# Performance work log

Hardware: AMD Instinct MI355X
Metric: run time of the kernel (lower is better)

Reference implementation:

```python
import jax, jax.numpy as jnp
import numpy as np
from jax.ops import segment_sum

N = 100000
E = 3200000
IN_DIM = 256
OUT_DIM = 64
LN_EPS = 1e-5
NEG_SLOPE = 0.01


def setup_inputs() -> dict:
    key = jax.random.key(0)
    k1, k2, k3, k4, k5 = jax.random.split(key, 5)
    x = jax.random.normal(k1, (N, IN_DIM), dtype=jnp.float32)
    edge_index = jax.random.randint(k2, (2, E), 0, N, dtype=jnp.int32)
    edge_weight = jax.random.uniform(k3, (E,), dtype=jnp.float32)
    # GCNConv params (glorot-ish scale) + LayerNorm params
    W = jax.random.normal(k4, (IN_DIM, OUT_DIM), dtype=jnp.float32) / np.sqrt(IN_DIM)
    b = jnp.zeros((OUT_DIM,), dtype=jnp.float32)
    gamma = jnp.ones((OUT_DIM,), dtype=jnp.float32)
    beta = jnp.zeros((OUT_DIM,), dtype=jnp.float32)
    return {"x": x, "edge_index": edge_index, "edge_weight": edge_weight,
            "W": W, "b": b, "gamma": gamma, "beta": beta}


def _gcn_forward(x, edge_index, edge_weight, W, b, gamma, beta):
    n = x.shape[0]
    # add self-loops with weight 1 (PyG GCNConv default)
    loops = jnp.arange(n, dtype=edge_index.dtype)
    src = jnp.concatenate([edge_index[0], loops])   # [E+N] message sources
    dst = jnp.concatenate([edge_index[1], loops])   # [E+N] aggregation targets
    ew = jnp.concatenate([edge_weight, jnp.ones((n,), dtype=edge_weight.dtype)])
    # symmetric normalization: deg computed on dst via weighted scatter
    deg = segment_sum(ew, dst, num_segments=n)                   # [N]
    dinv = jnp.where(deg > 0, jax.lax.rsqrt(deg), 0.0)           # deg^{-1/2}
    norm = dinv[src] * ew * dinv[dst]                            # [E+N]
    h = x @ W                                                    # [N, OUT]
    agg = segment_sum(h[src] * norm[:, None], dst, num_segments=n)  # [N, OUT]
    y = agg + b
    # leaky_relu then LayerNorm over last dim
    y = jnp.where(y >= 0, y, NEG_SLOPE * y)
    mu = jnp.mean(y, axis=-1, keepdims=True)
    var = jnp.mean(jnp.square(y - mu), axis=-1, keepdims=True)
    return (y - mu) * jax.lax.rsqrt(var + LN_EPS) * gamma + beta


def reference(x, edge_index, edge_weight, W, b, gamma, beta):
    return _gcn_forward(x, edge_index, edge_weight, W, b, gamma, beta)
```

## Files before the change

kernel.cpp:

```cpp
#include <hip/hip_runtime.h>

#define NN 100000
#define NE 3200000
#define OVCAP 65536

#define BINSZ 64
#define NBIN ((NN + BINSZ - 1) / BINSZ)
#define MAXPB 4096
#define SCAT_BLOCKS 512

struct OvEnt { int dst; int src; float ew; int pad; };


__global__ void k_zero(int* __restrict__ bincnt, int* __restrict__ ovcnt, int n) {
    int i = blockIdx.x * 256 + threadIdx.x;
    if (i < n) bincnt[i] = 0;
    if (i == 0) *ovcnt = 0;
}

__global__ __launch_bounds__(256) void k_binscatter(
    const int* __restrict__ src, const int* __restrict__ dst,
    const float* __restrict__ ew, int* __restrict__ bincnt,
    uint2* __restrict__ binbuf, int cap,
    OvEnt* __restrict__ ov, int* __restrict__ ovcnt, int e) {
    __shared__ int hist[NBIN];
    int t = threadIdx.x;
    int chunk = (e + gridDim.x - 1) / gridDim.x;
    int beg = blockIdx.x * chunk;
    int end = beg + chunk; if (end > e) end = e;
    for (int j = t; j < NBIN; j += 256) hist[j] = 0;
    __syncthreads();
    for (int i = beg + t; i < end; i += 256)
        atomicAdd(&hist[dst[i] >> 6], 1);
    __syncthreads();
    for (int j = t; j < NBIN; j += 256) {
        int c = hist[j];
        hist[j] = (c > 0) ? atomicAdd(&bincnt[j], c) : 0;
    }
    __syncthreads();
    for (int i = beg + t; i < end; i += 256) {
        int s = src[i], d = dst[i];
        float w = ew[i];
        int bin = d >> 6;
        int pos = atomicAdd(&hist[bin], 1);
        if (pos < cap) {
            unsigned key = (unsigned)s | ((unsigned)(d & 63) << 17);
            binbuf[(size_t)bin * cap + pos] = make_uint2(key, __float_as_uint(w));
        } else {
            int op = atomicAdd(ovcnt, 1);
            if (op < OVCAP) { OvEnt t2; t2.dst = d; t2.src = s; t2.ew = w; t2.pad = 0; ov[op] = t2; }
        }
    }
}

__global__ __launch_bounds__(256) void k_binsort(
    const int* __restrict__ bincnt, uint2* __restrict__ binbuf, int cap,
    const OvEnt* __restrict__ ov, const int* __restrict__ ovcnt,
    float* __restrict__ dinv, int* __restrict__ off, int* __restrict__ ncnt,
    int* __restrict__ binov, int n) {
    __shared__ float sdeg[BINSZ];
    __shared__ int hcnt[BINSZ];
    __shared__ int hoff[BINSZ];
    __shared__ int sov;
    __shared__ uint2 sbuf[MAXPB];
    int bin = blockIdx.x, t = threadIdx.x;
    if (t < BINSZ) { sdeg[t] = 0.f; hcnt[t] = 0; }
    if (t == 0) {
        int c = bincnt[bin];
        sov = (c > cap);
        binov[bin] = (c > cap);
    }
    __syncthreads();
    int cnt = bincnt[bin];
    int bc = cnt < cap ? cnt : cap;
    uint2* base = binbuf + (size_t)bin * cap;
    uint2 ent[16];
    int ne = 0;
#pragma unroll
    for (int p = 0; p < 16; p++) {
        int idx = t + p * 256;
        if (idx < bc) { ent[p] = base[idx]; ne = p + 1; }
    }
#pragma unroll
    for (int p = 0; p < 16; p++) {
        if (p < ne) {
            int dl = (int)((ent[p].x >> 17) & 63u);
            atomicAdd(&hcnt[dl], 1);
            atomicAdd(&sdeg[dl], __uint_as_float(ent[p].y));
        }
    }
    if (sov) {
        int on = *ovcnt; if (on > OVCAP) on = OVCAP;
        for (int j = t; j < on; j += 256) {
            OvEnt e2 = ov[j];
            if ((e2.dst >> 6) == bin) atomicAdd(&sdeg[e2.dst & 63], e2.ew);
        }
    }
    __syncthreads();
    if (t < 64) {
        int v = hcnt[t];
        int inc = v;
#pragma unroll
        for (int o2 = 1; o2 < 64; o2 <<= 1) {
            int u = __shfl_up(inc, o2, 64);
            if (t >= o2) inc += u;
        }
        int excl = inc - v;
        hoff[t] = excl;
        int g = bin * BINSZ + t;
        if (g < n) {
            dinv[g] = rsqrtf(1.0f + sdeg[t]);
            off[g] = bin * cap + excl;
            ncnt[g] = v;
        }
    }
    __syncthreads();
#pragma unroll
    for (int p = 0; p < 16; p++) {
        if (p < ne) {
            int dl = (int)((ent[p].x >> 17) & 63u);
            int pos = atomicAdd(&hoff[dl], 1);
            sbuf[pos] = ent[p];
        }
    }
    __syncthreads();
    for (int j = t; j < bc; j += 256) base[j] = sbuf[j];
}

__global__ __launch_bounds__(256) void k_gather_s(
    const float* __restrict__ h, const float* __restrict__ dinv,
    const int* __restrict__ binov,
    const int* __restrict__ off, const int* __restrict__ ncnt,
    const uint2* __restrict__ sorted,
    const OvEnt* __restrict__ ov, const int* __restrict__ ovcnt,
    const float* __restrict__ bias, const float* __restrict__ gamma,
    const float* __restrict__ beta, float* __restrict__ out, int n) {
    int lane = threadIdx.x & 63, wid = threadIdx.x >> 6;
    int node = blockIdx.x * 4 + wid;
    if (node >= n) return;
    float di = dinv[node];
    float acc = h[(size_t)node * 64 + lane] * di * di;
    int beg = off[node], c0 = ncnt[node];
    for (int j = 0; j < c0; j += 64) {
        int c = c0 - j; if (c > 64) c = 64;
        int s = 0; float w = 0.f;
        if (lane < c) {
            uint2 v = sorted[beg + j + lane];
            s = (int)(v.x & 0x1FFFFu);
            w = __uint_as_float(v.y) * dinv[s] * di;
        }
        int i2 = 0;
        for (; i2 + 16 <= c; i2 += 16) {
            float hv[16], wv[16];
#pragma unroll
            for (int q = 0; q < 16; q++) {
                int si = __shfl(s, i2 + q, 64);
                wv[q] = __shfl(w, i2 + q, 64);
                hv[q] = h[(size_t)si * 64 + lane];
            }
#pragma unroll
            for (int q = 0; q < 16; q++) acc += hv[q] * wv[q];
        }
        if (i2 < c) {
            float hv[16], wv[16];
            int rem = c - i2;
#pragma unroll
            for (int q = 0; q < 16; q++) {
                if (q < rem) {
                    int si = __shfl(s, i2 + q, 64);
                    wv[q] = __shfl(w, i2 + q, 64);
                    hv[q] = h[(size_t)si * 64 + lane];
                } else { wv[q] = 0.f; hv[q] = 0.f; }
            }
#pragma unroll
            for (int q = 0; q < 16; q++) acc += hv[q] * wv[q];
        }
    }
    if (binov[node >> 6]) {
        int on = *ovcnt; if (on > OVCAP) on = OVCAP;
        for (int j = 0; j < on; j++) {
            OvEnt ent = ov[j];
            if (ent.dst == node)
                acc += h[(size_t)ent.src * 64 + lane] * dinv[ent.src] * ent.ew * di;
        }
    }
    float y = acc + bias[lane];
    y = (y >= 0.f) ? y : 0.01f * y;
    float sum = y;
#pragma unroll
    for (int o = 32; o > 0; o >>= 1) sum += __shfl_xor(sum, o, 64);
    float mu = sum * (1.0f / 64.0f);
    float d = y - mu;
    float v = d * d;
#pragma unroll
    for (int o = 32; o > 0; o >>= 1) v += __shfl_xor(v, o, 64);
    v *= (1.0f / 64.0f);
    out[(size_t)node * 64 + lane] = d * rsqrtf(v + 1e-5f) * gamma[lane] + beta[lane];
}

#define GR 64
#define GKC 32
#define XS_STRIDE 36
__global__ __launch_bounds__(256) void k_gemm(const float* __restrict__ x,
                                              const float* __restrict__ W,
                                              float* __restrict__ h, int n) {
    __shared__ float xs[GR][XS_STRIDE];
    __shared__ float wsh[GKC][64];
    int t = threadIdx.x;
    int tx = t & 15;
    int ty = t >> 4;
    int rbase = blockIdx.x * GR;
    float acc[4][4];
#pragma unroll
    for (int i = 0; i < 4; i++)
#pragma unroll
        for (int j = 0; j < 4; j++) acc[i][j] = 0.0f;

    for (int k0 = 0; k0 < 256; k0 += GKC) {
        const float4* wsrc = (const float4*)(W + k0 * 64);
        float4* wdst = (float4*)(&wsh[0][0]);
        wdst[t] = wsrc[t];
        wdst[t + 256] = wsrc[t + 256];
#pragma unroll
        for (int p = 0; p < 2; p++) {
            int f4 = p * 256 + t;
            int r = f4 >> 3;
            int kq = (f4 & 7) << 2;
            int row = rbase + r;
            float4 val = make_float4(0.f, 0.f, 0.f, 0.f);
            if (row < n) val = *(const float4*)(x + (size_t)row * 256 + k0 + kq);
            *(float4*)(&xs[r][kq]) = val;
        }
        __syncthreads();
        int r0 = ty * 4, c0 = tx * 4;
#pragma unroll
        for (int kk = 0; kk < GKC; kk += 4) {
            float4 wv[4];
#pragma unroll
            for (int m = 0; m < 4; m++) wv[m] = *(const float4*)(&wsh[kk + m][c0]);
#pragma unroll
            for (int i = 0; i < 4; i++) {
                float4 xv = *(const float4*)(&xs[r0 + i][kk]);
                acc[i][0] += xv.x * wv[0].x + xv.y * wv[1].x + xv.z * wv[2].x + xv.w * wv[3].x;
                acc[i][1] += xv.x * wv[0].y + xv.y * wv[1].y + xv.z * wv[2].y + xv.w * wv[3].y;
                acc[i][2] += xv.x * wv[0].z + xv.y * wv[1].z + xv.z * wv[2].z + xv.w * wv[3].z;
                acc[i][3] += xv.x * wv[0].w + xv.y * wv[1].w + xv.z * wv[2].w + xv.w * wv[3].w;
            }
        }
        __syncthreads();
    }
    int r0 = ty * 4, c0 = tx * 4;
#pragma unroll
    for (int i = 0; i < 4; i++) {
        int row = rbase + r0 + i;
        if (row < n) {
            float4 v = make_float4(acc[i][0], acc[i][1], acc[i][2], acc[i][3]);
            *(float4*)(h + (size_t)row * 64 + c0) = v;
        }
    }
}


__global__ void k_init(float* __restrict__ deg, int* __restrict__ cnt, int n) {
    int i = blockIdx.x * 256 + threadIdx.x;
    if (i < n) { deg[i] = 1.0f; cnt[i] = 0; }
}

__global__ void k_deg(const int* __restrict__ dst, const float* __restrict__ ew,
                      float* __restrict__ deg, int* __restrict__ cnt, int e) {
    int i = blockIdx.x * 256 + threadIdx.x;
    if (i < e) {
        int d = dst[i];
        atomicAdd(&deg[d], ew[i]);
        atomicAdd(&cnt[d], 1);
    }
}

#define SCAN_T 256
#define SCAN_E 8
__global__ void k_scan_blocks(const int* __restrict__ cnt, int* __restrict__ off,
                              int* __restrict__ bsum, int n) {
    __shared__ int sdata[SCAN_T];
    int base = blockIdx.x * (SCAN_T * SCAN_E);
    int t = threadIdx.x;
    int v[SCAN_E];
    int local = 0;
    int idx0 = base + t * SCAN_E;
#pragma unroll
    for (int i = 0; i < SCAN_E; i++) {
        int idx = idx0 + i;
        int c = (idx < n) ? cnt[idx] : 0;
        v[i] = local;
        local += c;
    }
    sdata[t] = local;
    __syncthreads();
    for (int o = 1; o < SCAN_T; o <<= 1) {
        int x = 0;
        if (t >= o) x = sdata[t - o];
        __syncthreads();
        sdata[t] += x;
        __syncthreads();
    }
    int excl = sdata[t] - local;
#pragma unroll
    for (int i = 0; i < SCAN_E; i++) {
        int idx = idx0 + i;
        if (idx < n) off[idx] = excl + v[i];
    }
    if (t == SCAN_T - 1) bsum[blockIdx.x] = sdata[t];
}

__global__ void k_scan_bsums(int* __restrict__ bsum, int nb) {
    int t = threadIdx.x;
    int v = (t < nb) ? bsum[t] : 0;
    int orig = v;
#pragma unroll
    for (int o = 1; o < 64; o <<= 1) {
        int u = __shfl_up(v, o, 64);
        if (t >= o) v += u;
    }
    if (t < nb) bsum[t] = v - orig;
}

__global__ void k_finalize(int* __restrict__ off, const int* __restrict__ bsum,
                           int* __restrict__ cursor, float* __restrict__ deg,
                           int n, int total) {
    int i = blockIdx.x * 256 + threadIdx.x;
    if (i < n) {
        int o = off[i] + bsum[i >> 11];
        off[i] = o;
        cursor[i] = o;
        deg[i] = rsqrtf(deg[i]);
    }
    if (i == 0) off[n] = total;
}

__global__ void k_scatter(const int* __restrict__ src, const int* __restrict__ dst,
                          const float* __restrict__ ew, const float* __restrict__ dinv,
                          int* __restrict__ cursor, int* __restrict__ ssrc,
                          float* __restrict__ snorm, int e) {
    int i = blockIdx.x * 256 + threadIdx.x;
    if (i < e) {
        int s = src[i], d = dst[i];
        float nm = dinv[s] * ew[i] * dinv[d];
        int pos = atomicAdd(&cursor[d], 1);
        ssrc[pos] = s;
        snorm[pos] = nm;
    }
}

__global__ __launch_bounds__(256) void k_gather(
    const float* __restrict__ h, const float* __restrict__ dinv,
    const int* __restrict__ off, const int* __restrict__ ssrc,
    const float* __restrict__ snorm, const float* __restrict__ bias,
    const float* __restrict__ gamma, const float* __restrict__ beta,
    float* __restrict__ out, int n) {
    int lane = threadIdx.x & 63;
    int wid = threadIdx.x >> 6;
    int node = blockIdx.x * 4 + wid;
    if (node >= n) return;
    float di = dinv[node];
    float acc = h[(size_t)node * 64 + lane] * di * di;
    int beg = off[node], end = off[node + 1];
    for (int j = beg; j < end; j += 64) {
        int cnt = end - j;
        if (cnt > 64) cnt = 64;
        int s = 0;
        float w = 0.f;
        if (lane < cnt) { s = ssrc[j + lane]; w = snorm[j + lane]; }
        for (int i2 = 0; i2 < cnt; i2++) {
            int si = __shfl(s, i2, 64);
            float wi = __shfl(w, i2, 64);
            acc += h[(size_t)si * 64 + lane] * wi;
        }
    }
    float y = acc + bias[lane];
    y = (y >= 0.f) ? y : 0.01f * y;
    float sum = y;
#pragma unroll
    for (int o = 32; o > 0; o >>= 1) sum += __shfl_xor(sum, o, 64);
    float mu = sum * (1.0f / 64.0f);
    float d = y - mu;
    float v = d * d;
#pragma unroll
    for (int o = 32; o > 0; o >>= 1) v += __shfl_xor(v, o, 64);
    v *= (1.0f / 64.0f);
    out[(size_t)node * 64 + lane] = d * rsqrtf(v + 1e-5f) * gamma[lane] + beta[lane];
}


extern "C" void kernel_launch(void* const* d_in, const int* in_sizes, int n_in,
                              void* d_out, int out_size, void* d_ws, size_t ws_size,
                              hipStream_t stream) {
    const float* x = (const float*)d_in[0];
    const int* ei = (const int*)d_in[1];
    const float* ew = (const float*)d_in[2];
    const float* W = (const float*)d_in[3];
    const float* b = (const float*)d_in[4];
    const float* gamma = (const float*)d_in[5];
    const float* beta = (const float*)d_in[6];
    float* out = (float*)d_out;

    const int n = NN, e = NE;
    const int* src = ei;
    const int* dst = ei + e;

    char* ws = (char*)d_ws;
    size_t o = 0;
    auto alloc = [&](size_t bytes) -> char* {
        char* r = ws + o;
        o = (o + bytes + 255) & ~(size_t)255;
        return r;
    };
    auto pad = [](size_t bytes) -> size_t { return (bytes + 255) & ~(size_t)255; };

    int nb_n = (n + 255) / 256;
    int nb_e = (e + 255) / 256;
    int nb_gemm = (n + GR - 1) / GR;
    int nb_w = (n + 3) / 4;

    size_t fixed = 0;
    fixed += pad((size_t)NBIN * 4);
    fixed += 256;
    fixed += pad((size_t)OVCAP * 16);
    fixed += pad((size_t)n * 4);
    fixed += pad((size_t)n * 4);
    fixed += pad((size_t)n * 4);
    fixed += pad((size_t)NBIN * 4);
    fixed += pad((size_t)n * 64 * 4);

    int cap = 0;
    if (ws_size >= fixed + pad((size_t)NBIN * 4096 * 8) + 1024) cap = 4096;
    else if (ws_size >= fixed + pad((size_t)NBIN * 3072 * 8) + 1024) cap = 3072;

    if (cap > 0) {
        int* bincnt = (int*)alloc((size_t)NBIN * 4);
        int* ovcnt = (int*)alloc(4);
        OvEnt* ov = (OvEnt*)alloc((size_t)OVCAP * 16);
        float* dinv = (float*)alloc((size_t)n * 4);
        int* off = (int*)alloc((size_t)n * 4);
        int* ncnt = (int*)alloc((size_t)n * 4);
        int* binov = (int*)alloc((size_t)NBIN * 4);
        float* h = (float*)alloc((size_t)n * 64 * 4);
        uint2* binbuf = (uint2*)alloc((size_t)NBIN * cap * 8);

        int nb_z = (NBIN + 255) / 256;
        k_zero<<<nb_z, 256, 0, stream>>>(bincnt, ovcnt, NBIN);
        k_binscatter<<<SCAT_BLOCKS, 256, 0, stream>>>(src, dst, ew, bincnt, binbuf, cap,
                                                      ov, ovcnt, e);
        k_binsort<<<NBIN, 256, 0, stream>>>(bincnt, binbuf, cap, ov, ovcnt,
                                            dinv, off, ncnt, binov, n);
        k_gemm<<<nb_gemm, 256, 0, stream>>>(x, W, h, n);
        k_gather_s<<<nb_w, 256, 0, stream>>>(h, dinv, binov, off, ncnt, binbuf,
                                             ov, ovcnt, b, gamma, beta, out, n);
    } else {
        float* deg = (float*)alloc((size_t)n * 4);
        int* cnt = (int*)alloc((size_t)n * 4);
        int* off = (int*)alloc((size_t)(n + 1) * 4);
        int* cursor = (int*)alloc((size_t)n * 4);
        int* bsum = (int*)alloc(64 * 4);
        float* h = (float*)alloc((size_t)n * 64 * 4);
        int* ssrc = (int*)alloc((size_t)e * 4);
        float* snorm = (float*)alloc((size_t)e * 4);
        int nb_scan = (n + SCAN_T * SCAN_E - 1) / (SCAN_T * SCAN_E);

        k_init<<<nb_n, 256, 0, stream>>>(deg, cnt, n);
        k_deg<<<nb_e, 256, 0, stream>>>(dst, ew, deg, cnt, e);
        k_scan_blocks<<<nb_scan, SCAN_T, 0, stream>>>(cnt, off, bsum, n);
        k_scan_bsums<<<1, 64, 0, stream>>>(bsum, nb_scan);
        k_finalize<<<nb_n, 256, 0, stream>>>(off, bsum, cursor, deg, n, e);
        k_scatter<<<nb_e, 256, 0, stream>>>(src, dst, ew, deg, cursor, ssrc, snorm, e);
        k_gemm<<<nb_gemm, 256, 0, stream>>>(x, W, h, n);
        k_gather<<<nb_w, 256, 0, stream>>>(h, deg, off, ssrc, snorm, b, gamma, beta, out, n);
    }
}
```

Measured before the change: 470.8 us.

## Gather four edges per wave with float4 row loads in aggregation kernel

Rewrites the per-node gather so each wave processes four edges at once, with 16 lanes each loading a float4 slice of a source row, in place of one scalar per lane per edge after shuffling indices. Partial sums are combined with cross-quarter shuffles before the self-loop, bias, leaky-relu and LayerNorm epilogue, which also works on float4. Edge records are read with nontemporal loads and outputs written with nontemporal stores. The edge buffer gets a small padding because clamped or over-read indices may touch beyond the segment. The aim is fewer memory instructions and more loads in flight per edge. The cost is redundant work in the epilogue across the four quarters and wasted lanes on the tail of short edge lists.

```diff
diff --git a/kernel.cpp b/kernel.cpp
--- a/kernel.cpp
+++ b/kernel.cpp
@@ -138,64 +138,79 @@
     int lane = threadIdx.x & 63, wid = threadIdx.x >> 6;
     int node = blockIdx.x * 4 + wid;
     if (node >= n) return;
+    int qw = lane >> 4;
+    int cl = lane & 15;
+    const unsigned long long* sorted64 = (const unsigned long long*)sorted;
     float di = dinv[node];
-    float acc = h[(size_t)node * 64 + lane] * di * di;
     int beg = off[node], c0 = ncnt[node];
-    for (int j = 0; j < c0; j += 64) {
-        int c = c0 - j; if (c > 64) c = 64;
-        int s = 0; float w = 0.f;
-        if (lane < c) {
-            uint2 v = sorted[beg + j + lane];
-            s = (int)(v.x & 0x1FFFFu);
-            w = __uint_as_float(v.y) * dinv[s] * di;
-        }
-        int i2 = 0;
-        for (; i2 + 16 <= c; i2 += 16) {
-            float hv[16], wv[16];
-#pragma unroll
-            for (int q = 0; q < 16; q++) {
-                int si = __shfl(s, i2 + q, 64);
-                wv[q] = __shfl(w, i2 + q, 64);
-                hv[q] = h[(size_t)si * 64 + lane];
-            }
-#pragma unroll
-            for (int q = 0; q < 16; q++) acc += hv[q] * wv[q];
-        }
-        if (i2 < c) {
-            float hv[16], wv[16];
-            int rem = c - i2;
-#pragma unroll
-            for (int q = 0; q < 16; q++) {
-                if (q < rem) {
-                    int si = __shfl(s, i2 + q, 64);
-                    wv[q] = __shfl(w, i2 + q, 64);
-                    hv[q] = h[(size_t)si * 64 + lane];
-                } else { wv[q] = 0.f; hv[q] = 0.f; }
-            }
-#pragma unroll
-            for (int q = 0; q < 16; q++) acc += hv[q] * wv[q];
+    float ax = 0.f, ay = 0.f, az = 0.f, aw = 0.f;
+
+    for (int j = 0; j < c0; j += 32) {
+        float4 hv[8]; float wv[8];
+#pragma unroll
+        for (int q = 0; q < 8; q++) {
+            int ei = j + q * 4 + qw;
+            int eic = ei < c0 ? ei : (c0 ? c0 - 1 : 0);
+            unsigned long long v64 = __builtin_nontemporal_load(&sorted64[beg + eic]);
+            int s_ = (int)((unsigned)v64 & 0x1FFFFu);
+            wv[q] = (ei < c0) ? __uint_as_float((unsigned)(v64 >> 32)) * dinv[s_] * di : 0.f;
+            hv[q] = *(const float4*)(h + (size_t)s_ * 64 + (cl << 2));
+        }
+#pragma unroll
+        for (int q = 0; q < 8; q++) {
+            ax += hv[q].x * wv[q];
+            ay += hv[q].y * wv[q];
+            az += hv[q].z * wv[q];
+            aw += hv[q].w * wv[q];
         }
     }
     if (binov[node >> 6]) {
         int on = *ovcnt; if (on > OVCAP) on = OVCAP;
-        for (int j = 0; j < on; j++) {
-            OvEnt ent = ov[j];
-            if (ent.dst == node)
-                acc += h[(size_t)ent.src * 64 + lane] * dinv[ent.src] * ent.ew * di;
-        }
-    }
-    float y = acc + bias[lane];
-    y = (y >= 0.f) ? y : 0.01f * y;
-    float sum = y;
-#pragma unroll
-    for (int o = 32; o > 0; o >>= 1) sum += __shfl_xor(sum, o, 64);
-    float mu = sum * (1.0f / 64.0f);
-    float d = y - mu;
-    float v = d * d;
-#pragma unroll
-    for (int o = 32; o > 0; o >>= 1) v += __shfl_xor(v, o, 64);
-    v *= (1.0f / 64.0f);
-    out[(size_t)node * 64 + lane] = d * rsqrtf(v + 1e-5f) * gamma[lane] + beta[lane];
+        for (int j2 = 0; j2 < on; j2++) {
+            OvEnt ent = ov[j2];
+            if (ent.dst == node && qw == 0) {
+                float w_ = ent.ew * dinv[ent.src] * di;
+                float4 hq = *(const float4*)(h + (size_t)ent.src * 64 + (cl << 2));
+                ax += hq.x * w_; ay += hq.y * w_; az += hq.z * w_; aw += hq.w * w_;
+            }
+        }
+    }
+    ax += __shfl_xor(ax, 16, 64); ax += __shfl_xor(ax, 32, 64);
+    ay += __shfl_xor(ay, 16, 64); ay += __shfl_xor(ay, 32, 64);
+    az += __shfl_xor(az, 16, 64); az += __shfl_xor(az, 32, 64);
+    aw += __shfl_xor(aw, 16, 64); aw += __shfl_xor(aw, 32, 64);
+
+    float4 hs = *(const float4*)(h + (size_t)node * 64 + (cl << 2));
+    float4 b4 = *(const float4*)(bias + (cl << 2));
+    float dd = di * di;
+    float yx = ax + hs.x * dd + b4.x;
+    float yy = ay + hs.y * dd + b4.y;
+    float yz = az + hs.z * dd + b4.z;
+    float yw = aw + hs.w * dd + b4.w;
+    yx = (yx >= 0.f) ? yx : 0.01f * yx;
+    yy = (yy >= 0.f) ? yy : 0.01f * yy;
+    yz = (yz >= 0.f) ? yz : 0.01f * yz;
+    yw = (yw >= 0.f) ? yw : 0.01f * yw;
+
+    float s1 = yx + yy + yz + yw;
+    s1 += __shfl_xor(s1, 1, 64); s1 += __shfl_xor(s1, 2, 64);
+    s1 += __shfl_xor(s1, 4, 64); s1 += __shfl_xor(s1, 8, 64);
+    float mu = s1 * (1.0f / 64.0f);
+    float dx = yx - mu, dy = yy - mu, dz = yz - mu, dw = yw - mu;
+    float v1 = dx * dx + dy * dy + dz * dz + dw * dw;
+    v1 += __shfl_xor(v1, 1, 64); v1 += __shfl_xor(v1, 2, 64);
+    v1 += __shfl_xor(v1, 4, 64); v1 += __shfl_xor(v1, 8, 64);
+    v1 *= (1.0f / 64.0f);
+    float inv = rsqrtf(v1 + 1e-5f);
+    float4 g4 = *(const float4*)(gamma + (cl << 2));
+    float4 be4 = *(const float4*)(beta + (cl << 2));
+    if (qw == 0) {
+        float* op = out + (size_t)node * 64 + (cl << 2);
+        __builtin_nontemporal_store(dx * inv * g4.x + be4.x, op + 0);
+        __builtin_nontemporal_store(dy * inv * g4.y + be4.y, op + 1);
+        __builtin_nontemporal_store(dz * inv * g4.z + be4.z, op + 2);
+        __builtin_nontemporal_store(dw * inv * g4.w + be4.w, op + 3);
+    }
 }
 
 #define GR 64
@@ -431,8 +446,8 @@
     fixed += pad((size_t)n * 64 * 4);
 
     int cap = 0;
-    if (ws_size >= fixed + pad((size_t)NBIN * 4096 * 8) + 1024) cap = 4096;
-    else if (ws_size >= fixed + pad((size_t)NBIN * 3072 * 8) + 1024) cap = 3072;
+    if (ws_size >= fixed + pad((size_t)NBIN * 4096 * 8 + 4096) + 8192) cap = 4096;
+    else if (ws_size >= fixed + pad((size_t)NBIN * 3072 * 8 + 4096) + 8192) cap = 3072;
 
     if (cap > 0) {
         int* bincnt = (int*)alloc((size_t)NBIN * 4);
@@ -443,7 +458,7 @@
         int* ncnt = (int*)alloc((size_t)n * 4);
         int* binov = (int*)alloc((size_t)NBIN * 4);
         float* h = (float*)alloc((size_t)n * 64 * 4);
-        uint2* binbuf = (uint2*)alloc((size_t)NBIN * cap * 8);
+        uint2* binbuf = (uint2*)alloc((size_t)NBIN * cap * 8 + 4096);
 
         int nb_z = (NBIN + 255) / 256;
         k_zero<<<nb_z, 256, 0, stream>>>(bincnt, ovcnt, NBIN);
```

After: 528.5 us. 12.2% more time.
